# Kernel tuning notes

Measured on AMD Instinct MI355X. Metric: run time of the kernel, lower is better.

## Reference

```python
import jax, jax.numpy as jnp
import numpy as np

WINDOW = (6, 7, 7)  # (agent_size, window_size, window_size)
HEADS = 8           # dim // dim_head = 256 // 32


def _relative_position_index(ws):
    d, h, w = ws
    coords = np.stack(np.meshgrid(np.arange(d), np.arange(h), np.arange(w), indexing='ij'))
    cf = coords.reshape(3, -1)                      # [3, n]
    rel = cf[:, :, None] - cf[:, None, :]           # [3, n, n]
    rel = rel.transpose(1, 2, 0).copy()             # [n, n, 3]
    rel[..., 0] += d - 1
    rel[..., 1] += h - 1
    rel[..., 2] += w - 1
    rel[..., 0] *= (2 * h - 1) * (2 * w - 1)
    rel[..., 1] *= (2 * w - 1)
    return rel.sum(-1)                              # [n, n] int

REL_IDX = jnp.asarray(_relative_position_index(WINDOW))


def setup_inputs() -> dict:
    key = jax.random.key(0)
    ks = jax.random.split(key, 7)
    dim = 256
    n_bias = (2 * WINDOW[0] - 1) * (2 * WINDOW[1] - 1) * (2 * WINDOW[2] - 1)  # 1859
    s = 0.02
    return {
        'x': jax.random.normal(ks[0], (2, 6, 12, 12, 7, 7, dim), jnp.float32),
        'Wq': jax.random.normal(ks[1], (dim, dim), jnp.float32) * s,
        'bq': jax.random.normal(ks[2], (dim,), jnp.float32) * s,
        'Wkv': jax.random.normal(ks[3], (dim, 2 * dim), jnp.float32) * s,
        'bkv': jax.random.normal(ks[4], (2 * dim,), jnp.float32) * s,
        'Wout': jax.random.normal(ks[5], (dim, dim), jnp.float32) * s,
        'bias_table': jax.random.normal(ks[6], (n_bias, HEADS), jnp.float32) * s,
    }


def reference(x, Wq, bq, Wkv, bkv, Wout, bias_table):
    b, l, gx, gy, w1, w2, d = x.shape
    h = HEADS
    dh = d // h
    n = l * w1 * w2
    B = b * gx * gy
    # 'b l x y w1 w2 d -> (b x y) (l w1 w2) d'  (agent-major token order)
    xt = jnp.transpose(x, (0, 2, 3, 1, 4, 5, 6)).reshape(B, n, d)
    q = xt @ Wq + bq                                  # [B, n, d]
    kv = xt @ Wkv + bkv                               # [B, n, 2d]
    k, v = kv[..., :d], kv[..., d:]
    split = lambda t: t.reshape(B, n, h, dh).transpose(0, 2, 1, 3)  # [B, h, n, dh]
    q, k, v = split(q), split(k), split(v)
    scale = dh ** -0.5
    sim = jnp.einsum('bhid,bhjd->bhij', q * scale, k)  # [B, h, n, n]
    bias = bias_table[REL_IDX]                         # [n, n, h]
    sim = sim + jnp.transpose(bias, (2, 0, 1))[None]
    attn = jax.nn.softmax(sim, axis=-1)
    out = jnp.einsum('bhij,bhjd->bhid', attn, v)       # [B, h, n, dh]
    out = out.transpose(0, 2, 1, 3).reshape(B, n, d) @ Wout
    # '(b x y) (l w1 w2) d -> b l x y w1 w2 d'
    out = out.reshape(b, gx, gy, l, w1, w2, d)
    return jnp.transpose(out, (0, 3, 1, 2, 4, 5, 6))
```

## Files before the change

### kernel.cpp

```cpp
#include <hip/hip_runtime.h>
#include <hip/hip_bf16.h>

#define DIM    256
#define NWIN   294
#define BWIN   288
#define MROWS  (BWIN * NWIN)
#define MPAD   84736
#define NHEADS 8
#define DH     32
#define NBIAS  1859
#define QPAD   304

typedef __attribute__((ext_vector_type(8))) short  short8;
typedef __attribute__((ext_vector_type(4))) float  f32x4;

__device__ __forceinline__ unsigned short f2bf(float f) {
    unsigned int u = __float_as_uint(f);
    u += 0x7FFFu + ((u >> 16) & 1u);
    return (unsigned short)(u >> 16);
}

__device__ __forceinline__ unsigned pk2bf(float a, float b) {
    __hip_bfloat162 h = __float22bfloat162_rn(float2{a, b});
    unsigned u;
    __builtin_memcpy(&u, &h, 4);
    return u;
}

__device__ __forceinline__ void gl_lds16(const void* g, void* l) {
    __builtin_amdgcn_global_load_lds((const __attribute__((address_space(1))) unsigned int*)g,
                                     (__attribute__((address_space(3))) unsigned int*)l,
                                     16, 0, 0);
}

__device__ __forceinline__ int xcd_swizzle(int orig, int nwg) {
    const int xcd = orig & 7, idx = orig >> 3;
    const int q = nwg >> 3, r = nwg & 7;
    return (xcd < r) ? (xcd * (q + 1) + idx) : (r * (q + 1) + (xcd - r) * q + idx);
}

__device__ __forceinline__ void stage_tile(const unsigned short* aBase, const unsigned short* bBase,
                                           unsigned short* As_, unsigned short* Bs_, int w, int k0)
{
#pragma unroll
    for (int i = 0; i < 4; ++i) {
        const int c = w * 4 + i;
        gl_lds16(aBase + (size_t)c * 8 * 256 + k0, As_ + c * 512);
        gl_lds16(bBase + (size_t)c * 8 * 256 + k0, Bs_ + c * 512);
    }
}

__device__ __forceinline__ void tile_mfma(const unsigned short* As_, const unsigned short* Bs_,
                                          int wm, int wn, int quad, int l15, f32x4 (&acc)[4][4])
{
#pragma unroll
    for (int c2 = 0; c2 < 2; ++c2) {
        const int kk = c2 * 32 + quad * 8;
        short8 a[4], b[4];
#pragma unroll
        for (int mi = 0; mi < 4; ++mi)
            a[mi] = *(const short8*)&As_[(wm * 64 + mi * 16 + l15) * 64 + kk];
#pragma unroll
        for (int ni = 0; ni < 4; ++ni)
            b[ni] = *(const short8*)&Bs_[(wn * 64 + ni * 16 + l15) * 64 + kk];
#pragma unroll
        for (int mi = 0; mi < 4; ++mi)
#pragma unroll
            for (int ni = 0; ni < 4; ++ni)
                acc[mi][ni] = __builtin_amdgcn_mfma_f32_16x16x32_bf16(a[mi], b[ni], acc[mi][ni], 0, 0, 0);
    }
}

__global__ __launch_bounds__(256) void prep_x(const float* __restrict__ x,
                                              unsigned short* __restrict__ Xb)
{
    const int g   = blockIdx.x * 256 + threadIdx.x;
    const int row = g >> 5;
    const int col = (g & 31) * 8;
    if (row >= MPAD) return;
    uint4 pk;
    if (row < MROWS) {
        const int bw = row / NWIN, rw = row - bw * NWIN;
        const int bb = bw / 144,  r2 = bw - bb * 144;
        const int gxi = r2 / 12,  gyi = r2 - gxi * 12;
        const int lz = rw / 49,   r3 = rw - lz * 49;
        const int wa = r3 / 7,    wb = r3 - wa * 7;
        const float* src = x + ((((((size_t)bb * 6 + lz) * 12 + gxi) * 12 + gyi) * 7 + wa) * 7 + wb) * DIM + col;
        const float4 f0 = *(const float4*)(src);
        const float4 f1 = *(const float4*)(src + 4);
        pk.x = pk2bf(f0.x, f0.y);
        pk.y = pk2bf(f0.z, f0.w);
        pk.z = pk2bf(f1.x, f1.y);
        pk.w = pk2bf(f1.z, f1.w);
    } else {
        pk = (uint4){0u, 0u, 0u, 0u};
    }
    *(uint4*)(Xb + (size_t)row * 256 + col) = pk;
}

__global__ __launch_bounds__(256) void prep_w(const float* __restrict__ Wq,
                                              const float* __restrict__ Wkv,
                                              const float* __restrict__ Wout,
                                              unsigned short* __restrict__ Wt,
                                              unsigned short* __restrict__ Wot)
{
    const int g = blockIdx.x * 256 + threadIdx.x;
    if (g < 768 * 256) {
        const int n = g >> 8, k = g & 255;
        const float v = (n < 256) ? Wq[k * 256 + n] : Wkv[k * 512 + (n - 256)];
        Wt[g] = f2bf(v);
    } else {
        const int g2 = g - 768 * 256;
        const int n = g2 >> 8, k = g2 & 255;
        Wot[g2] = f2bf(Wout[k * 256 + n]);
    }
}

__global__ __launch_bounds__(256) void prep_bias(const float* __restrict__ bias_table,
                                                 float* __restrict__ biasT)
{
    const int g = blockIdx.x * 256 + threadIdx.x;
    if (g >= NHEADS * QPAD * QPAD) return;
    const int k = g % QPAD;
    const int q = (g / QPAD) % QPAD;
    const int h = g / (QPAD * QPAD);
    float v = 0.f;
    if (q < NWIN && k < NWIN) {
        const int ql = q / 49, qr = q - ql * 49, qa = qr / 7, qb = qr - qa * 7;
        const int kl = k / 49, kr = k - kl * 49, ka = kr / 7, kb = kr - ka * 7;
        const int idx = 169 * (ql - kl + 5) + 13 * (qa - ka + 6) + (qb - kb + 6);
        v = bias_table[idx * NHEADS + h] * 1.44269504088896f;
    }
    biasT[g] = v;
}

__global__ __launch_bounds__(256) void gemm_qkv(
    const unsigned short* __restrict__ Xb, const unsigned short* __restrict__ Wt,
    const float* __restrict__ bq, const float* __restrict__ bkv,
    unsigned short* __restrict__ Qb, unsigned short* __restrict__ Kb,
    unsigned short* __restrict__ Vtb)
{
    __shared__ __align__(16) unsigned short As[2][128 * 64];
    __shared__ __align__(16) unsigned short Bs[2][128 * 64];

    const int wg = xcd_swizzle(blockIdx.x, 662 * 6);
    const int bn = wg % 6;
    const int bm = wg / 6;
    const int tileM = bm * 128;
    const int tileN = bn * 128;

    const int t    = threadIdx.x;
    const int w    = t >> 6;
    const int lane = t & 63;
    const int quad = lane >> 4;
    const int l15  = lane & 15;
    const int wm   = w >> 1, wn = w & 1;

    const int rA = lane >> 3;
    const int kA = (lane & 7) * 8;
    const unsigned short* aBase = Xb + ((size_t)tileM + rA) * 256 + kA;
    const unsigned short* bBase = Wt + ((size_t)tileN + rA) * 256 + kA;

    f32x4 acc[4][4] = {};

    stage_tile(aBase, bBase, As[0], Bs[0], w, 0);
    __syncthreads();
#pragma unroll
    for (int kb = 0; kb < 3; ++kb) {
        const int cur = kb & 1;
        stage_tile(aBase, bBase, As[cur ^ 1], Bs[cur ^ 1], w, (kb + 1) * 64);
        tile_mfma(As[cur], Bs[cur], wm, wn, quad, l15, acc);
        __syncthreads();
    }
    tile_mfma(As[1], Bs[1], wm, wn, quad, l15, acc);

    const int colB = tileN + wn * 64;
    float bias[4];
#pragma unroll
    for (int ni = 0; ni < 4; ++ni) {
        const int n = colB + ni * 16 + l15;
        bias[ni] = (n < 256) ? bq[n] : bkv[n - 256];
    }
    const int rowB = tileM + wm * 64 + quad * 4;
#pragma unroll
    for (int mi = 0; mi < 4; ++mi) {
        const int row0 = rowB + mi * 16;
        if (row0 < MROWS) {
            const int bw0 = row0 / NWIN;
            const int rw0 = row0 - bw0 * NWIN;
            const bool same = (rw0 <= NWIN - 4);
#pragma unroll
            for (int ni = 0; ni < 4; ++ni) {
                const int n = colB + ni * 16 + l15;
                const int ch = n & 255;
                const int hd = ch >> 5, di = ch & 31;
                if (n < 512) {
                    unsigned short* dst = (n < 256) ? Qb : Kb;
                    if (same) {
                        unsigned short* p = dst + ((size_t)(bw0 * NHEADS + hd) * NWIN + rw0) * DH + di;
#pragma unroll
                        for (int r = 0; r < 4; ++r)
                            p[r * DH] = f2bf(acc[mi][ni][r] + bias[ni]);
                    } else {
#pragma unroll
                        for (int r = 0; r < 4; ++r) {
                            const int row = row0 + r;
                            if (row < MROWS) {
                                const int bw = row / NWIN, rw = row - bw * NWIN;
                                dst[((size_t)(bw * NHEADS + hd) * NWIN + rw) * DH + di] =
                                    f2bf(acc[mi][ni][r] + bias[ni]);
                            }
                        }
                    }
                } else {
                    if (same) {
                        unsigned short* p = Vtb + ((size_t)(bw0 * NHEADS + hd) * DH + di) * NWIN + rw0;
                        const unsigned lo = pk2bf(acc[mi][ni][0] + bias[ni], acc[mi][ni][1] + bias[ni]);
                        const unsigned hi = pk2bf(acc[mi][ni][2] + bias[ni], acc[mi][ni][3] + bias[ni]);
                        *(unsigned*)(p)     = lo;
                        *(unsigned*)(p + 2) = hi;
                    } else {
#pragma unroll
                        for (int r = 0; r < 4; ++r) {
                            const int row = row0 + r;
                            if (row < MROWS) {
                                const int bw = row / NWIN, rw = row - bw * NWIN;
                                Vtb[((size_t)(bw * NHEADS + hd) * DH + di) * NWIN + rw] =
                                    f2bf(acc[mi][ni][r] + bias[ni]);
                            }
                        }
                    }
                }
            }
        }
    }
}

__global__ __launch_bounds__(256, 3) void attn_kernel(
    const unsigned short* __restrict__ Qb, const unsigned short* __restrict__ Kb,
    const unsigned short* __restrict__ Vtb, const float* __restrict__ biasT,
    unsigned short* __restrict__ Ob)
{
    const int bh   = blockIdx.x;
    const int bwin = bh >> 3;
    const int h    = bh & 7;

    __shared__ __align__(16) unsigned short Ks[304 * 40];
    __shared__ __align__(16) unsigned short Vts[32 * 328];

    const int t    = threadIdx.x;
    const int w    = t >> 6;
    const int lane = t & 63;
    const int quad = lane >> 4;
    const int l15  = lane & 15;

    {
        const unsigned short* Kg = Kb + (size_t)bh * (NWIN * DH);
        for (int i = t; i < 304 * 4; i += 256) {
            const int row = i >> 2, seg = i & 3;
            uint4 v = (uint4){0u, 0u, 0u, 0u};
            if (row < NWIN) v = *(const uint4*)(Kg + row * 32 + seg * 8);
            *(uint4*)(Ks + row * 40 + seg * 8) = v;
        }
    }
    {
        const unsigned short* Vg = Vtb + (size_t)bh * (DH * NWIN);
        for (int i = t; i < 32 * 80; i += 256) {
            const int d = i / 80, c = i - d * 80;
            const int kt = c >> 3, qd = (c >> 1) & 3, hf = c & 1;
            const int kb = kt * 32 + hf * 16 + qd * 4;
            unsigned int u0 = 0u, u1 = 0u;
            if (kb + 3 < NWIN) {
                u0 = *(const unsigned int*)(Vg + d * NWIN + kb);
                u1 = *(const unsigned int*)(Vg + d * NWIN + kb + 2);
            } else if (kb < NWIN) {
                unsigned short r0 = Vg[d * NWIN + kb];
                unsigned short r1 = (kb + 1 < NWIN) ? Vg[d * NWIN + kb + 1] : (unsigned short)0;
                unsigned short r2 = (kb + 2 < NWIN) ? Vg[d * NWIN + kb + 2] : (unsigned short)0;
                u0 = (unsigned int)r0 | ((unsigned int)r1 << 16);
                u1 = (unsigned int)r2;
            }
            unsigned int* dst = (unsigned int*)(Vts + d * 328 + c * 4);
            dst[0] = u0; dst[1] = u1;
        }
    }
    __syncthreads();

    const float SL2E = 0.25503486f;
    const unsigned short* Qg = Qb + (size_t)bh * (NWIN * DH);
    const float* biasH = biasT + (size_t)h * QPAD * QPAD;
    const short8 ones = (short8){0x3F80,0x3F80,0x3F80,0x3F80,0x3F80,0x3F80,0x3F80,0x3F80};

#pragma unroll
    for (int r5 = 0; r5 < 5; ++r5) {
        const int it = 4 * r5 + w;
        if (it < 19) {
            short8 qf;
            const int qrow = it * 16 + l15;
            if (qrow < NWIN) qf = *(const short8*)(Qg + qrow * DH + quad * 8);
            else             qf = (short8){0,0,0,0,0,0,0,0};

            const float* bb = biasH + (size_t)qrow * QPAD;

            f32x4 S[19];
#pragma unroll
            for (int jt = 0; jt < 19; ++jt) {
                const short8 kf = *(const short8*)(Ks + (jt * 16 + l15) * 40 + quad * 8);
                S[jt] = __builtin_amdgcn_mfma_f32_16x16x32_bf16(kf, qf, (f32x4){0.f,0.f,0.f,0.f}, 0, 0, 0);
            }

            unsigned pk0[20], pk1[20];
            pk0[19] = 0u; pk1[19] = 0u;
#pragma unroll
            for (int jt = 0; jt < 19; ++jt) {
                const f32x4 b4 = *(const f32x4*)(bb + jt * 16 + quad * 4);
                float p0 = exp2f(fmaf(S[jt][0], SL2E, b4[0]));
                float p1 = exp2f(fmaf(S[jt][1], SL2E, b4[1]));
                float p2 = exp2f(fmaf(S[jt][2], SL2E, b4[2]));
                float p3 = exp2f(fmaf(S[jt][3], SL2E, b4[3]));
                if (jt == 18) {
                    if (quad * 4 + 0 >= 6) p0 = 0.f;
                    if (quad * 4 + 1 >= 6) p1 = 0.f;
                    if (quad * 4 + 2 >= 6) p2 = 0.f;
                    if (quad * 4 + 3 >= 6) p3 = 0.f;
                }
                pk0[jt] = pk2bf(p0, p1);
                pk1[jt] = pk2bf(p2, p3);
            }

            f32x4 o0 = {0.f,0.f,0.f,0.f}, o1 = {0.f,0.f,0.f,0.f}, o2 = {0.f,0.f,0.f,0.f};
#pragma unroll
            for (int kt = 0; kt < 10; ++kt) {
                uint4 pw;
                pw.x = pk0[2 * kt];
                pw.y = pk1[2 * kt];
                pw.z = pk0[2 * kt + 1];
                pw.w = pk1[2 * kt + 1];
                short8 pa;
                __builtin_memcpy(&pa, &pw, 16);
                const short8 v0 = *(const short8*)(Vts + l15 * 328 + kt * 32 + quad * 8);
                const short8 v1 = *(const short8*)(Vts + (16 + l15) * 328 + kt * 32 + quad * 8);
                o0 = __builtin_amdgcn_mfma_f32_16x16x32_bf16(pa, v0, o0, 0, 0, 0);
                o1 = __builtin_amdgcn_mfma_f32_16x16x32_bf16(pa, v1, o1, 0, 0, 0);
                o2 = __builtin_amdgcn_mfma_f32_16x16x32_bf16(pa, ones, o2, 0, 0, 0);
            }

#pragma unroll
            for (int r = 0; r < 4; ++r) {
                const int rg = it * 16 + quad * 4 + r;
                if (rg < NWIN) {
                    const float inv = 1.0f / o2[r];
                    unsigned short* op = Ob + ((size_t)bwin * NWIN + rg) * DIM + h * DH;
                    op[l15]      = f2bf(o0[r] * inv);
                    op[16 + l15] = f2bf(o1[r] * inv);
                }
            }
        }
    }
}

__global__ __launch_bounds__(256) void gemm_out(
    const unsigned short* __restrict__ Ob, const unsigned short* __restrict__ Wot,
    float* __restrict__ out)
{
    __shared__ __align__(16) unsigned short As[2][128 * 64];
    __shared__ __align__(16) unsigned short Bs[2][128 * 64];

    const int wg = xcd_swizzle(blockIdx.x, 662 * 2);
    const int bn = wg & 1;
    const int bm = wg >> 1;
    const int tileM = bm * 128;
    const int tileN = bn * 128;

    const int t    = threadIdx.x;
    const int w    = t >> 6;
    const int lane = t & 63;
    const int quad = lane >> 4;
    const int l15  = lane & 15;
    const int wm   = w >> 1, wn = w & 1;

    const int rA = lane >> 3;
    const int kA = (lane & 7) * 8;
    const unsigned short* aBase = Ob  + ((size_t)tileM + rA) * 256 + kA;
    const unsigned short* bBase = Wot + ((size_t)tileN + rA) * 256 + kA;

    f32x4 acc[4][4] = {};

    stage_tile(aBase, bBase, As[0], Bs[0], w, 0);
    __syncthreads();
#pragma unroll
    for (int kb = 0; kb < 3; ++kb) {
        const int cur = kb & 1;
        stage_tile(aBase, bBase, As[cur ^ 1], Bs[cur ^ 1], w, (kb + 1) * 64);
        tile_mfma(As[cur], Bs[cur], wm, wn, quad, l15, acc);
        __syncthreads();
    }
    tile_mfma(As[1], Bs[1], wm, wn, quad, l15, acc);

    const int colB = tileN + wn * 64;
    const int rowB = tileM + wm * 64 + quad * 4;
#pragma unroll
    for (int mi = 0; mi < 4; ++mi) {
#pragma unroll
        for (int r = 0; r < 4; ++r) {
            const int row = rowB + mi * 16 + r;
            if (row < MROWS) {
                const int bw = row / NWIN, rw = row - bw * NWIN;
                const int bb = bw / 144,  r2 = bw - bb * 144;
                const int gxi = r2 / 12,  gyi = r2 - gxi * 12;
                const int lz = rw / 49,   r3 = rw - lz * 49;
                const int wa = r3 / 7,    wb = r3 - wa * 7;
                float* orow = out + ((((((size_t)bb * 6 + lz) * 12 + gxi) * 12 + gyi) * 7 + wa) * 7 + wb) * DIM;
#pragma unroll
                for (int ni = 0; ni < 4; ++ni)
                    orow[colB + ni * 16 + l15] = acc[mi][ni][r];
            }
        }
    }
}

extern "C" void kernel_launch(void* const* d_in, const int* in_sizes, int n_in,
                              void* d_out, int out_size, void* d_ws, size_t ws_size,
                              hipStream_t stream)
{
    const float* x          = (const float*)d_in[0];
    const float* Wq         = (const float*)d_in[1];
    const float* bq         = (const float*)d_in[2];
    const float* Wkv        = (const float*)d_in[3];
    const float* bkv        = (const float*)d_in[4];
    const float* Wout       = (const float*)d_in[5];
    const float* bias_table = (const float*)d_in[6];
    float* out = (float*)d_out;

    const size_t planePad = (size_t)MPAD * DIM;
    const size_t plane    = (size_t)MROWS * DIM;
    unsigned short* Xb  = (unsigned short*)d_ws;
    unsigned short* Qb  = Xb + planePad;
    unsigned short* Kb  = Qb + plane;
    unsigned short* Vtb = Kb + plane;
    unsigned short* Ob  = Vtb + plane;
    unsigned short* Wt  = Ob + planePad;
    unsigned short* Wot = Wt + 768 * 256;
    float*          biasT = (float*)(Wot + 256 * 256);

    prep_x<<<MPAD / 8, 256, 0, stream>>>(x, Xb);
    prep_w<<<1024, 256, 0, stream>>>(Wq, Wkv, Wout, Wt, Wot);
    prep_bias<<<(NHEADS * QPAD * QPAD + 255) / 256, 256, 0, stream>>>(bias_table, biasT);
    gemm_qkv<<<662 * 6, 256, 0, stream>>>(Xb, Wt, bq, bkv, Qb, Kb, Vtb);
    attn_kernel<<<BWIN * NHEADS, 256, 0, stream>>>(Qb, Kb, Vtb, biasT, Ob);
    gemm_out<<<662 * 2, 256, 0, stream>>>(Ob, Wot, out);
}
```

Baseline: 375.2 us.

## Read K fragments directly from padded global memory instead of staging in LDS

K is now written by the QKV GEMM into a per-(window,head) buffer padded to 304 rows, and a new small kernel zeroes the 10 pad rows. The attention kernel drops its K staging loop into shared memory and loads MFMA K fragments straight from global/L2, which frees LDS. It also removes the occupancy hint of 3 blocks per CU from the launch bounds. This trades LDS traffic and a staging pass for repeated global loads of K by each wave, whose cost depends on cache hit rates.

```diff
diff --git a/kernel.cpp b/kernel.cpp
--- a/kernel.cpp
+++ b/kernel.cpp
@@ -10,6 +10,8 @@
 #define DH     32
 #define NBIAS  1859
 #define QPAD   304
+#define KPAD   304
+#define KPITCH (KPAD * DH)
 
 typedef __attribute__((ext_vector_type(8))) short  short8;
 typedef __attribute__((ext_vector_type(4))) float  f32x4;
@@ -134,6 +136,14 @@
     biasT[g] = v;
 }
 
+__global__ __launch_bounds__(256) void prep_zero(unsigned short* __restrict__ Kb)
+{
+    const int g = blockIdx.x * 256 + threadIdx.x;
+    if (g >= BWIN * NHEADS * 40) return;
+    const int bh = g / 40, r = g - bh * 40;
+    *(uint4*)(Kb + (size_t)bh * KPITCH + NWIN * DH + r * 8) = (uint4){0u, 0u, 0u, 0u};
+}
+
 __global__ __launch_bounds__(256) void gemm_qkv(
     const unsigned short* __restrict__ Xb, const unsigned short* __restrict__ Wt,
     const float* __restrict__ bq, const float* __restrict__ bkv,
@@ -194,10 +204,9 @@
                 const int n = colB + ni * 16 + l15;
                 const int ch = n & 255;
                 const int hd = ch >> 5, di = ch & 31;
-                if (n < 512) {
-                    unsigned short* dst = (n < 256) ? Qb : Kb;
+                if (n < 256) {
                     if (same) {
-                        unsigned short* p = dst + ((size_t)(bw0 * NHEADS + hd) * NWIN + rw0) * DH + di;
+                        unsigned short* p = Qb + ((size_t)(bw0 * NHEADS + hd) * NWIN + rw0) * DH + di;
 #pragma unroll
                         for (int r = 0; r < 4; ++r)
                             p[r * DH] = f2bf(acc[mi][ni][r] + bias[ni]);
@@ -207,7 +216,24 @@
                             const int row = row0 + r;
                             if (row < MROWS) {
                                 const int bw = row / NWIN, rw = row - bw * NWIN;
-                                dst[((size_t)(bw * NHEADS + hd) * NWIN + rw) * DH + di] =
+                                Qb[((size_t)(bw * NHEADS + hd) * NWIN + rw) * DH + di] =
+                                    f2bf(acc[mi][ni][r] + bias[ni]);
+                            }
+                        }
+                    }
+                } else if (n < 512) {
+                    if (same) {
+                        unsigned short* p = Kb + ((size_t)(bw0 * NHEADS + hd) * KPAD + rw0) * DH + di;
+#pragma unroll
+                        for (int r = 0; r < 4; ++r)
+                            p[r * DH] = f2bf(acc[mi][ni][r] + bias[ni]);
+                    } else {
+#pragma unroll
+                        for (int r = 0; r < 4; ++r) {
+                            const int row = row0 + r;
+                            if (row < MROWS) {
+                                const int bw = row / NWIN, rw = row - bw * NWIN;
+                                Kb[((size_t)(bw * NHEADS + hd) * KPAD + rw) * DH + di] =
                                     f2bf(acc[mi][ni][r] + bias[ni]);
                             }
                         }
@@ -236,7 +262,7 @@
     }
 }
 
-__global__ __launch_bounds__(256, 3) void attn_kernel(
+__global__ __launch_bounds__(256) void attn_kernel(
     const unsigned short* __restrict__ Qb, const unsigned short* __restrict__ Kb,
     const unsigned short* __restrict__ Vtb, const float* __restrict__ biasT,
     unsigned short* __restrict__ Ob)
@@ -245,7 +271,6 @@
     const int bwin = bh >> 3;
     const int h    = bh & 7;
 
-    __shared__ __align__(16) unsigned short Ks[304 * 40];
     __shared__ __align__(16) unsigned short Vts[32 * 328];
 
     const int t    = threadIdx.x;
@@ -254,15 +279,6 @@
     const int quad = lane >> 4;
     const int l15  = lane & 15;
 
-    {
-        const unsigned short* Kg = Kb + (size_t)bh * (NWIN * DH);
-        for (int i = t; i < 304 * 4; i += 256) {
-            const int row = i >> 2, seg = i & 3;
-            uint4 v = (uint4){0u, 0u, 0u, 0u};
-            if (row < NWIN) v = *(const uint4*)(Kg + row * 32 + seg * 8);
-            *(uint4*)(Ks + row * 40 + seg * 8) = v;
-        }
-    }
     {
         const unsigned short* Vg = Vtb + (size_t)bh * (DH * NWIN);
         for (int i = t; i < 32 * 80; i += 256) {
@@ -288,6 +304,7 @@
 
     const float SL2E = 0.25503486f;
     const unsigned short* Qg = Qb + (size_t)bh * (NWIN * DH);
+    const unsigned short* Kg = Kb + (size_t)bh * KPITCH;
     const float* biasH = biasT + (size_t)h * QPAD * QPAD;
     const short8 ones = (short8){0x3F80,0x3F80,0x3F80,0x3F80,0x3F80,0x3F80,0x3F80,0x3F80};
 
@@ -305,7 +322,7 @@
             f32x4 S[19];
 #pragma unroll
             for (int jt = 0; jt < 19; ++jt) {
-                const short8 kf = *(const short8*)(Ks + (jt * 16 + l15) * 40 + quad * 8);
+                const short8 kf = *(const short8*)(Kg + (jt * 16 + l15) * DH + quad * 8);
                 S[jt] = __builtin_amdgcn_mfma_f32_16x16x32_bf16(kf, qf, (f32x4){0.f,0.f,0.f,0.f}, 0, 0, 0);
             }
 
@@ -434,10 +451,11 @@
 
     const size_t planePad = (size_t)MPAD * DIM;
     const size_t plane    = (size_t)MROWS * DIM;
+    const size_t planeK   = (size_t)BWIN * NHEADS * KPITCH;
     unsigned short* Xb  = (unsigned short*)d_ws;
     unsigned short* Qb  = Xb + planePad;
     unsigned short* Kb  = Qb + plane;
-    unsigned short* Vtb = Kb + plane;
+    unsigned short* Vtb = Kb + planeK;
     unsigned short* Ob  = Vtb + plane;
     unsigned short* Wt  = Ob + planePad;
     unsigned short* Wot = Wt + 768 * 256;
@@ -446,6 +464,7 @@
     prep_x<<<MPAD / 8, 256, 0, stream>>>(x, Xb);
     prep_w<<<1024, 256, 0, stream>>>(Wq, Wkv, Wout, Wt, Wot);
     prep_bias<<<(NHEADS * QPAD * QPAD + 255) / 256, 256, 0, stream>>>(bias_table, biasT);
+    prep_zero<<<(BWIN * NHEADS * 40 + 255) / 256, 256, 0, stream>>>(Kb);
     gemm_qkv<<<662 * 6, 256, 0, stream>>>(Xb, Wt, bq, bkv, Qb, Kb, Vtb);
     attn_kernel<<<BWIN * NHEADS, 256, 0, stream>>>(Qb, Kb, Vtb, biasT, Ob);
     gemm_out<<<662 * 2, 256, 0, stream>>>(Ob, Wot, out);
```

Measured after the change: 421.2 us. +12.3%, slower.

## Fuse x transpose and bf16 conversion into QKV GEMM A-tile staging

Applied to the files above, without the earlier changes.

Removes the separate prep_x kernel and the bf16 staging buffer. The QKV GEMM now loads fp32 x directly with the window permutation, converts it to bf16 in registers and writes it to LDS. This drops one launch and a full intermediate write and read. In exchange, each x row is read in fp32 by every N-tile block, and A staging loses the asynchronous global-to-LDS path.

```diff
diff --git a/kernel.cpp b/kernel.cpp
--- a/kernel.cpp
+++ b/kernel.cpp
@@ -39,13 +39,12 @@
     return (xcd < r) ? (xcd * (q + 1) + idx) : (r * (q + 1) + (xcd - r) * q + idx);
 }
 
-__device__ __forceinline__ void stage_tile(const unsigned short* aBase, const unsigned short* bBase,
-                                           unsigned short* As_, unsigned short* Bs_, int w, int k0)
+__device__ __forceinline__ void stage_b(const unsigned short* bBase,
+                                        unsigned short* Bs_, int w, int k0)
 {
 #pragma unroll
     for (int i = 0; i < 4; ++i) {
         const int c = w * 4 + i;
-        gl_lds16(aBase + (size_t)c * 8 * 256 + k0, As_ + c * 512);
         gl_lds16(bBase + (size_t)c * 8 * 256 + k0, Bs_ + c * 512);
     }
 }
@@ -69,33 +68,6 @@
             for (int ni = 0; ni < 4; ++ni)
                 acc[mi][ni] = __builtin_amdgcn_mfma_f32_16x16x32_bf16(a[mi], b[ni], acc[mi][ni], 0, 0, 0);
     }
-}
-
-__global__ __launch_bounds__(256) void prep_x(const float* __restrict__ x,
-                                              unsigned short* __restrict__ Xb)
-{
-    const int g   = blockIdx.x * 256 + threadIdx.x;
-    const int row = g >> 5;
-    const int col = (g & 31) * 8;
-    if (row >= MPAD) return;
-    uint4 pk;
-    if (row < MROWS) {
-        const int bw = row / NWIN, rw = row - bw * NWIN;
-        const int bb = bw / 144,  r2 = bw - bb * 144;
-        const int gxi = r2 / 12,  gyi = r2 - gxi * 12;
-        const int lz = rw / 49,   r3 = rw - lz * 49;
-        const int wa = r3 / 7,    wb = r3 - wa * 7;
-        const float* src = x + ((((((size_t)bb * 6 + lz) * 12 + gxi) * 12 + gyi) * 7 + wa) * 7 + wb) * DIM + col;
-        const float4 f0 = *(const float4*)(src);
-        const float4 f1 = *(const float4*)(src + 4);
-        pk.x = pk2bf(f0.x, f0.y);
-        pk.y = pk2bf(f0.z, f0.w);
-        pk.z = pk2bf(f1.x, f1.y);
-        pk.w = pk2bf(f1.z, f1.w);
-    } else {
-        pk = (uint4){0u, 0u, 0u, 0u};
-    }
-    *(uint4*)(Xb + (size_t)row * 256 + col) = pk;
 }
 
 __global__ __launch_bounds__(256) void prep_w(const float* __restrict__ Wq,
@@ -135,7 +107,7 @@
 }
 
 __global__ __launch_bounds__(256) void gemm_qkv(
-    const unsigned short* __restrict__ Xb, const unsigned short* __restrict__ Wt,
+    const float* __restrict__ x, const unsigned short* __restrict__ Wt,
     const float* __restrict__ bq, const float* __restrict__ bkv,
     unsigned short* __restrict__ Qb, unsigned short* __restrict__ Kb,
     unsigned short* __restrict__ Vtb)
@@ -158,17 +130,52 @@
 
     const int rA = lane >> 3;
     const int kA = (lane & 7) * 8;
-    const unsigned short* aBase = Xb + ((size_t)tileM + rA) * 256 + kA;
     const unsigned short* bBase = Wt + ((size_t)tileN + rA) * 256 + kA;
 
+    const float* xsrc[4];
+#pragma unroll
+    for (int i = 0; i < 4; ++i) {
+        const int row = tileM + (w * 4 + i) * 8 + rA;
+        if (row < MROWS) {
+            const int bw = row / NWIN, rw = row - bw * NWIN;
+            const int bb = bw / 144,  r2 = bw - bb * 144;
+            const int gxi = r2 / 12,  gyi = r2 - gxi * 12;
+            const int lz = rw / 49,   r3 = rw - lz * 49;
+            const int wa = r3 / 7,    wb = r3 - wa * 7;
+            xsrc[i] = x + ((((((size_t)bb * 6 + lz) * 12 + gxi) * 12 + gyi) * 7 + wa) * 7 + wb) * DIM + kA;
+        } else {
+            xsrc[i] = nullptr;
+        }
+    }
+
+    auto stage_a = [&](unsigned short* As_, int k0) {
+#pragma unroll
+        for (int i = 0; i < 4; ++i) {
+            uint4 pk;
+            if (xsrc[i]) {
+                const float4 f0 = *(const float4*)(xsrc[i] + k0);
+                const float4 f1 = *(const float4*)(xsrc[i] + k0 + 4);
+                pk.x = pk2bf(f0.x, f0.y);
+                pk.y = pk2bf(f0.z, f0.w);
+                pk.z = pk2bf(f1.x, f1.y);
+                pk.w = pk2bf(f1.z, f1.w);
+            } else {
+                pk = (uint4){0u, 0u, 0u, 0u};
+            }
+            *(uint4*)(As_ + (w * 4 + i) * 512 + lane * 8) = pk;
+        }
+    };
+
     f32x4 acc[4][4] = {};
 
-    stage_tile(aBase, bBase, As[0], Bs[0], w, 0);
+    stage_a(As[0], 0);
+    stage_b(bBase, Bs[0], w, 0);
     __syncthreads();
 #pragma unroll
     for (int kb = 0; kb < 3; ++kb) {
         const int cur = kb & 1;
-        stage_tile(aBase, bBase, As[cur ^ 1], Bs[cur ^ 1], w, (kb + 1) * 64);
+        stage_a(As[cur ^ 1], (kb + 1) * 64);
+        stage_b(bBase, Bs[cur ^ 1], w, (kb + 1) * 64);
         tile_mfma(As[cur], Bs[cur], wm, wn, quad, l15, acc);
         __syncthreads();
     }
@@ -386,12 +393,22 @@
 
     f32x4 acc[4][4] = {};
 
-    stage_tile(aBase, bBase, As[0], Bs[0], w, 0);
+#pragma unroll
+    for (int i = 0; i < 4; ++i) {
+        const int c = w * 4 + i;
+        gl_lds16(aBase + (size_t)c * 8 * 256, As[0] + c * 512);
+    }
+    stage_b(bBase, Bs[0], w, 0);
     __syncthreads();
 #pragma unroll
     for (int kb = 0; kb < 3; ++kb) {
         const int cur = kb & 1;
-        stage_tile(aBase, bBase, As[cur ^ 1], Bs[cur ^ 1], w, (kb + 1) * 64);
+#pragma unroll
+        for (int i = 0; i < 4; ++i) {
+            const int c = w * 4 + i;
+            gl_lds16(aBase + (size_t)c * 8 * 256 + (kb + 1) * 64, As[cur ^ 1] + c * 512);
+        }
+        stage_b(bBase, Bs[cur ^ 1], w, (kb + 1) * 64);
         tile_mfma(As[cur], Bs[cur], wm, wn, quad, l15, acc);
         __syncthreads();
     }
@@ -434,8 +451,7 @@
 
     const size_t planePad = (size_t)MPAD * DIM;
     const size_t plane    = (size_t)MROWS * DIM;
-    unsigned short* Xb  = (unsigned short*)d_ws;
-    unsigned short* Qb  = Xb + planePad;
+    unsigned short* Qb  = (unsigned short*)d_ws;
     unsigned short* Kb  = Qb + plane;
     unsigned short* Vtb = Kb + plane;
     unsigned short* Ob  = Vtb + plane;
@@ -443,10 +459,9 @@
     unsigned short* Wot = Wt + 768 * 256;
     float*          biasT = (float*)(Wot + 256 * 256);
 
-    prep_x<<<MPAD / 8, 256, 0, stream>>>(x, Xb);
     prep_w<<<1024, 256, 0, stream>>>(Wq, Wkv, Wout, Wt, Wot);
     prep_bias<<<(NHEADS * QPAD * QPAD + 255) / 256, 256, 0, stream>>>(bias_table, biasT);
-    gemm_qkv<<<662 * 6, 256, 0, stream>>>(Xb, Wt, bq, bkv, Qb, Kb, Vtb);
+    gemm_qkv<<<662 * 6, 256, 0, stream>>>(x, Wt, bq, bkv, Qb, Kb, Vtb);
     attn_kernel<<<BWIN * NHEADS, 256, 0, stream>>>(Qb, Kb, Vtb, biasT, Ob);
     gemm_out<<<662 * 2, 256, 0, stream>>>(Ob, Wot, out);
 }
```

After: 440.6 us. 1.17x slower.
